# Optimization experiments

Measured on AMD Instinct MI355X. Metric: run time of the kernel, lower is better.

Reference implementation:

```python
import jax, jax.numpy as jnp
import numpy as np

B = 8192      # sessions
L = 64        # tokens per session
T = B * L     # total tokens
H = 128       # hidden_size
MAX_LEN = 64  # position_emb has MAX_LEN+1 rows


def setup_inputs() -> dict:
    key = jax.random.key(0)
    ks = jax.random.split(key, 10)
    s1 = 1.0 / np.sqrt(H)
    s2 = 1.0 / np.sqrt(2 * H)
    hidden = jax.random.normal(ks[0], (T, H), jnp.float32)
    seq_len = jnp.full((B,), L, dtype=jnp.int32)
    # reversed positions 1..L within each session (<= MAX_LEN)
    reverse_pos = jnp.tile(jnp.arange(L, 0, -1, dtype=jnp.int32), B)
    return {
        "hidden": hidden,
        "pos_table": jax.random.normal(ks[1], (MAX_LEN + 1, H), jnp.float32) * 0.02,
        "W_pos_w": jax.random.normal(ks[2], (H, 2 * H), jnp.float32) * s2,
        "W_pos_b": jax.random.normal(ks[3], (H,), jnp.float32) * s2,
        "W1_w": jax.random.normal(ks[4], (H, H), jnp.float32) * s1,
        "W1_b": jax.random.normal(ks[5], (H,), jnp.float32) * s1,
        "W2_w": jax.random.normal(ks[6], (H, H), jnp.float32) * s1,
        "W2_b": jax.random.normal(ks[7], (H,), jnp.float32) * s1,
        "q_w": jax.random.normal(ks[8], (1, H), jnp.float32) * s1,
        "q_b": jax.random.normal(ks[9], (1,), jnp.float32) * s1,
        "seq_len": seq_len,
        "reverse_pos": reverse_pos,
    }


def reference(hidden, pos_table, W_pos_w, W_pos_b, W1_w, W1_b, W2_w, W2_b,
              q_w, q_b, seq_len, reverse_pos):
    Bn = seq_len.shape[0]
    Tn = hidden.shape[0]
    # token -> session id (replaces the python split loop)
    seg = jnp.repeat(jnp.arange(Bn), seq_len, total_repeat_length=Tn)  # [T]
    # per-session mean, broadcast back to tokens (v_mean_repeat_concat)
    mean = jax.ops.segment_sum(hidden, seg, num_segments=Bn) \
        / seq_len[:, None].astype(hidden.dtype)                        # [B,H]
    mean_rep = mean[seg]                                               # [T,H]
    pos_emb = pos_table[reverse_pos]                                   # [T,H]
    pos_hidden = jnp.tanh(
        jnp.concatenate([hidden, pos_emb], axis=-1) @ W_pos_w.T + W_pos_b
    )                                                                  # [T,H]
    gate = jax.nn.sigmoid(mean_rep @ W1_w.T + W1_b + pos_hidden @ W2_w.T + W2_b)
    alpha = gate @ q_w.T + q_b                                         # [T,1]
    # per-session sum of alpha-weighted tokens (h_s)
    return jax.ops.segment_sum(alpha * hidden, seg, num_segments=Bn)   # [B,H]
```

## Files before the change

kernel.cpp:

```cpp
#include <hip/hip_runtime.h>
#include <hip/hip_bf16.h>

typedef unsigned short u16;
typedef __bf16 bf16x8 __attribute__((ext_vector_type(8)));
typedef float  f32x4  __attribute__((ext_vector_type(4)));

__device__ __forceinline__ unsigned pk2(float a, float b) {
    __hip_bfloat162 h = __float22bfloat162_rn(make_float2(a, b));
    unsigned u; __builtin_memcpy(&u, &h, 4);
    return u;
}
__device__ __forceinline__ u16 f2b1(float f) { return (u16)(pk2(f, f) & 0xFFFFu); }

#define MFMA __builtin_amdgcn_mfma_f32_16x16x32_bf16

__global__ __launch_bounds__(128) void prep_kernel(
    const float* __restrict__ pos_table, const float* __restrict__ Wpw,
    const float* __restrict__ Wpb, const float* __restrict__ W2,
    float* __restrict__ ppK, u16* __restrict__ wb1, u16* __restrict__ wb2)
{
    const int b = blockIdx.x, t = threadIdx.x;
    if (b < 65) {
        const float4* pr = (const float4*)(pos_table + b * 128);
        const float4* wr = (const float4*)(Wpw + t * 256 + 128);
        float acc = Wpb[t];
        #pragma unroll
        for (int k = 0; k < 32; ++k) {
            const float4 p = pr[k], wv = wr[k];
            acc += p.x * wv.x + p.y * wv.y + p.z * wv.z + p.w * wv.w;
        }
        ppK[b * 128 + t] = acc * 2.885390081777927f;
    } else {
        const int j = b - 65;
        wb1[j * 128 + t] = f2b1(Wpw[j * 256 + t]);
        wb2[j * 128 + t] = f2b1(W2[j * 128 + t]);
    }
}

__global__ __launch_bounds__(256, 2) void fused_kernel(
    const float* __restrict__ hidden, const int* __restrict__ rpos,
    const float* __restrict__ W1, const float* __restrict__ W1b,
    const float* __restrict__ W2b, const float* __restrict__ qw,
    const float* __restrict__ qb, const float* __restrict__ ppK,
    const u16* __restrict__ wb1g, const u16* __restrict__ wb2g,
    float* __restrict__ out)
{
    __shared__ __align__(16) u16 hbf[128 * 136];
    __shared__ __align__(16) u16 wb[128 * 136];
    __shared__ float meanv[256];
    __shared__ float g1s[256];
    __shared__ float qws[128];
    __shared__ float alphas[128];
    __shared__ int   rps[128];

    const int tid = threadIdx.x;
    const int blk = blockIdx.x;
    const int w = tid >> 6;
    const int l = tid & 63;
    const int c = l & 15;
    const int g = l >> 4;
    const int R = 32 * w;
    const float* hsrc = hidden + (size_t)blk * (128 * 128);

    meanv[tid] = 0.f;
    if (tid < 128) { rps[tid] = rpos[blk * 128 + tid]; qws[tid] = qw[tid]; }
    __syncthreads();

    {
        float4 ms0 = {0.f, 0.f, 0.f, 0.f}, ms1 = {0.f, 0.f, 0.f, 0.f};
        #pragma unroll
        for (int i = 0; i < 16; ++i) {
            const int i4 = tid + i * 256;
            const float4 v = ((const float4*)hsrc)[i4];
            const int e = i4 * 4, row = e >> 7, col = e & 127;
            uint2 st; st.x = pk2(v.x, v.y); st.y = pk2(v.z, v.w);
            *(uint2*)&hbf[row * 136 + col] = st;
            if (i < 8) { ms0.x += v.x; ms0.y += v.y; ms0.z += v.z; ms0.w += v.w; }
            else       { ms1.x += v.x; ms1.y += v.y; ms1.z += v.z; ms1.w += v.w; }
        }
        const int mc = (tid * 4) & 127;
        atomicAdd(&meanv[mc],           ms0.x); atomicAdd(&meanv[mc + 1],       ms0.y);
        atomicAdd(&meanv[mc + 2],       ms0.z); atomicAdd(&meanv[mc + 3],       ms0.w);
        atomicAdd(&meanv[128 + mc],     ms1.x); atomicAdd(&meanv[128 + mc + 1], ms1.y);
        atomicAdd(&meanv[128 + mc + 2], ms1.z); atomicAdd(&meanv[128 + mc + 3], ms1.w);
    }
    #pragma unroll
    for (int i = 0; i < 8; ++i) {
        const int ch = tid + i * 256;
        const int e = ch * 8, row = e >> 7, col = e & 127;
        *(uint4*)&wb[row * 136 + col] = ((const uint4*)wb1g)[ch];
    }
    __syncthreads();

    {
        const int col = tid & 127, s = tid >> 7;
        const float4* wr = (const float4*)(W1 + col * 128);
        const float4* mv = (const float4*)(meanv + s * 128);
        float acc = 0.f;
        #pragma unroll 8
        for (int k4 = 0; k4 < 32; ++k4) {
            const float4 wv = wr[k4], m4 = mv[k4];
            acc += m4.x * wv.x + m4.y * wv.y + m4.z * wv.z + m4.w * wv.w;
        }
        g1s[tid] = W1b[col] + W2b[col] + acc * (1.f / 64.f);
    }

    bf16x8 af[2][4];
    #pragma unroll
    for (int m = 0; m < 2; ++m)
        #pragma unroll
        for (int kk = 0; kk < 4; ++kk)
            af[m][kk] = *(const bf16x8*)&hbf[(R + 16 * m + c) * 136 + kk * 32 + g * 8];
    f32x4 acc1[2][8] = {};
    #pragma unroll
    for (int n = 0; n < 8; ++n) {
        #pragma unroll
        for (int kk = 0; kk < 4; ++kk) {
            const bf16x8 bfr = *(const bf16x8*)&wb[(16 * n + c) * 136 + kk * 32 + g * 8];
            acc1[0][n] = MFMA(af[0][kk], bfr, acc1[0][n], 0, 0, 0);
            acc1[1][n] = MFMA(af[1][kk], bfr, acc1[1][n], 0, 0, 0);
        }
    }
    {
        const float K2 = 2.885390081777927f;
        const float* pkp[2][4];
        #pragma unroll
        for (int m = 0; m < 2; ++m)
            #pragma unroll
            for (int r = 0; r < 4; ++r)
                pkp[m][r] = ppK + rps[R + 16 * m + 4 * g + r] * 128 + c;
        #pragma unroll
        for (int m = 0; m < 2; ++m)
            #pragma unroll
            for (int n = 0; n < 8; ++n)
                #pragma unroll
                for (int r = 0; r < 4; ++r) {
                    const float arg = fmaf(acc1[m][n][r], K2, pkp[m][r][16 * n]);
                    const float e2 = __builtin_amdgcn_exp2f(arg);
                    const float rc = __builtin_amdgcn_rcpf(e2 + 1.f);
                    const float th = fmaf(-2.f, rc, 1.f);
                    hbf[(R + 16 * m + 4 * g + r) * 136 + 16 * n + c] = f2b1(th);
                }
    }
    __syncthreads();

    bf16x8 af2[2][4];
    #pragma unroll
    for (int m = 0; m < 2; ++m)
        #pragma unroll
        for (int kk = 0; kk < 4; ++kk)
            af2[m][kk] = *(const bf16x8*)&hbf[(R + 16 * m + c) * 136 + kk * 32 + g * 8];
    #pragma unroll
    for (int i = 0; i < 8; ++i) {
        const int ch = tid + i * 256;
        const int e = ch * 8, row = e >> 7, col = e & 127;
        *(uint4*)&wb[row * 136 + col] = ((const uint4*)wb2g)[ch];
    }
    __syncthreads();

    f32x4 acc2[2][8] = {};
    #pragma unroll
    for (int n = 0; n < 8; ++n) {
        #pragma unroll
        for (int kk = 0; kk < 4; ++kk) {
            const bf16x8 bfr = *(const bf16x8*)&wb[(16 * n + c) * 136 + kk * 32 + g * 8];
            acc2[0][n] = MFMA(af2[0][kk], bfr, acc2[0][n], 0, 0, 0);
            acc2[1][n] = MFMA(af2[1][kk], bfr, acc2[1][n], 0, 0, 0);
        }
    }
    {
        const float K1 = 1.4426950408889634f;
        const int sw = w >> 1;
        float garr[8], qarr[8];
        #pragma unroll
        for (int n = 0; n < 8; ++n) {
            garr[n] = -K1 * g1s[sw * 128 + 16 * n + c];
            qarr[n] = qws[16 * n + c];
        }
        float prt[2][4] = {};
        #pragma unroll
        for (int m = 0; m < 2; ++m)
            #pragma unroll
            for (int n = 0; n < 8; ++n)
                #pragma unroll
                for (int r = 0; r < 4; ++r) {
                    const float arg = fmaf(acc2[m][n][r], -K1, garr[n]);
                    const float e2 = __builtin_amdgcn_exp2f(arg);
                    const float rc = __builtin_amdgcn_rcpf(e2 + 1.f);
                    prt[m][r] = fmaf(rc, qarr[n], prt[m][r]);
                }
        #pragma unroll
        for (int msk = 1; msk <= 8; msk <<= 1)
            #pragma unroll
            for (int m = 0; m < 2; ++m)
                #pragma unroll
                for (int r = 0; r < 4; ++r)
                    prt[m][r] += __shfl_xor(prt[m][r], msk, 64);
        if (c == 0) {
            const float qbv = qb[0];
            #pragma unroll
            for (int m = 0; m < 2; ++m)
                #pragma unroll
                for (int r = 0; r < 4; ++r)
                    alphas[R + 16 * m + 4 * g + r] = prt[m][r] + qbv;
        }
    }
    __syncthreads();

    {
        const int h = tid & 127, p = tid >> 7;
        const float* hs = hsrc + p * (64 * 128) + h;
        float accf = 0.f;
        #pragma unroll 8
        for (int t = 0; t < 64; ++t)
            accf = fmaf(alphas[64 * p + t], hs[t * 128], accf);
        out[(size_t)blk * 256 + tid] = accf;
    }
}

extern "C" void kernel_launch(void* const* d_in, const int* in_sizes, int n_in,
                              void* d_out, int out_size, void* d_ws, size_t ws_size,
                              hipStream_t stream)
{
    const float* hidden    = (const float*)d_in[0];
    const float* pos_table = (const float*)d_in[1];
    const float* Wpw       = (const float*)d_in[2];
    const float* Wpb       = (const float*)d_in[3];
    const float* W1w       = (const float*)d_in[4];
    const float* W1b       = (const float*)d_in[5];
    const float* W2w       = (const float*)d_in[6];
    const float* W2b       = (const float*)d_in[7];
    const float* qw        = (const float*)d_in[8];
    const float* qb        = (const float*)d_in[9];
    const int*   rpos      = (const int*)d_in[11];
    float* out = (float*)d_out;

    const int B = in_sizes[10];

    char* wsb = (char*)d_ws;
    float* ppK = (float*)wsb;
    u16* wb1   = (u16*)(wsb + 33280);
    u16* wb2   = (u16*)(wsb + 33280 + 32768);

    prep_kernel<<<193, 128, 0, stream>>>(pos_table, Wpw, Wpb, W2w,
                                         ppK, wb1, wb2);
    fused_kernel<<<B / 2, 256, 0, stream>>>(hidden, rpos, W1w, W1b, W2b, qw, qb,
                                            ppK, wb1, wb2, out);
}
```

Measured before the change: 486.2 us.

## Double threads per block to 512 with 16-row MFMA tiles per wave

Raises the fused kernel block from 256 to 512 threads (8 waves), so each wave owns 16 token rows instead of 32 and per-thread register arrays shrink. The final weighted reduction is split into half-sessions and combined through shared memory. The mean accumulation uses a wave shuffle before fewer LDS atomics, and W2 bf16 weights are prefetched into registers early rather than loaded after the first GEMM. The aim is more latency hiding and occupancy; the cost is one extra barrier and more threads contending for the same LDS footprint.

```diff
diff --git a/kernel.cpp b/kernel.cpp
--- a/kernel.cpp
+++ b/kernel.cpp
@@ -37,7 +37,7 @@
     }
 }
 
-__global__ __launch_bounds__(256, 2) void fused_kernel(
+__global__ __launch_bounds__(512, 4) void fused_kernel(
     const float* __restrict__ hidden, const int* __restrict__ rpos,
     const float* __restrict__ W1, const float* __restrict__ W1b,
     const float* __restrict__ W2b, const float* __restrict__ qw,
@@ -47,7 +47,7 @@
 {
     __shared__ __align__(16) u16 hbf[128 * 136];
     __shared__ __align__(16) u16 wb[128 * 136];
-    __shared__ float meanv[256];
+    __shared__ __align__(16) float scratch[512];
     __shared__ float g1s[256];
     __shared__ float qws[128];
     __shared__ float alphas[128];
@@ -59,43 +59,51 @@
     const int l = tid & 63;
     const int c = l & 15;
     const int g = l >> 4;
-    const int R = 32 * w;
+    const int R = 16 * w;
     const float* hsrc = hidden + (size_t)blk * (128 * 128);
 
-    meanv[tid] = 0.f;
+    scratch[tid] = 0.f;
     if (tid < 128) { rps[tid] = rpos[blk * 128 + tid]; qws[tid] = qw[tid]; }
     __syncthreads();
 
+    uint4 wreg[4];
     {
         float4 ms0 = {0.f, 0.f, 0.f, 0.f}, ms1 = {0.f, 0.f, 0.f, 0.f};
         #pragma unroll
-        for (int i = 0; i < 16; ++i) {
-            const int i4 = tid + i * 256;
+        for (int i = 0; i < 8; ++i) {
+            const int i4 = tid + i * 512;
             const float4 v = ((const float4*)hsrc)[i4];
-            const int e = i4 * 4, row = e >> 7, col = e & 127;
+            const int row = i4 >> 5, col = (i4 * 4) & 127;
             uint2 st; st.x = pk2(v.x, v.y); st.y = pk2(v.z, v.w);
             *(uint2*)&hbf[row * 136 + col] = st;
-            if (i < 8) { ms0.x += v.x; ms0.y += v.y; ms0.z += v.z; ms0.w += v.w; }
+            if (i < 4) { ms0.x += v.x; ms0.y += v.y; ms0.z += v.z; ms0.w += v.w; }
             else       { ms1.x += v.x; ms1.y += v.y; ms1.z += v.z; ms1.w += v.w; }
         }
-        const int mc = (tid * 4) & 127;
-        atomicAdd(&meanv[mc],           ms0.x); atomicAdd(&meanv[mc + 1],       ms0.y);
-        atomicAdd(&meanv[mc + 2],       ms0.z); atomicAdd(&meanv[mc + 3],       ms0.w);
-        atomicAdd(&meanv[128 + mc],     ms1.x); atomicAdd(&meanv[128 + mc + 1], ms1.y);
-        atomicAdd(&meanv[128 + mc + 2], ms1.z); atomicAdd(&meanv[128 + mc + 3], ms1.w);
-    }
-    #pragma unroll
-    for (int i = 0; i < 8; ++i) {
-        const int ch = tid + i * 256;
-        const int e = ch * 8, row = e >> 7, col = e & 127;
+        ms0.x += __shfl_xor(ms0.x, 32, 64); ms0.y += __shfl_xor(ms0.y, 32, 64);
+        ms0.z += __shfl_xor(ms0.z, 32, 64); ms0.w += __shfl_xor(ms0.w, 32, 64);
+        ms1.x += __shfl_xor(ms1.x, 32, 64); ms1.y += __shfl_xor(ms1.y, 32, 64);
+        ms1.z += __shfl_xor(ms1.z, 32, 64); ms1.w += __shfl_xor(ms1.w, 32, 64);
+        if (l < 32) {
+            const int mc = 4 * l;
+            atomicAdd(&scratch[mc],           ms0.x); atomicAdd(&scratch[mc + 1],       ms0.y);
+            atomicAdd(&scratch[mc + 2],       ms0.z); atomicAdd(&scratch[mc + 3],       ms0.w);
+            atomicAdd(&scratch[128 + mc],     ms1.x); atomicAdd(&scratch[128 + mc + 1], ms1.y);
+            atomicAdd(&scratch[128 + mc + 2], ms1.z); atomicAdd(&scratch[128 + mc + 3], ms1.w);
+        }
+    }
+    #pragma unroll
+    for (int i = 0; i < 4; ++i) {
+        const int ch = tid + i * 512;
+        const int row = ch >> 4, col = (ch * 8) & 127;
         *(uint4*)&wb[row * 136 + col] = ((const uint4*)wb1g)[ch];
-    }
-    __syncthreads();
-
-    {
+        wreg[i] = ((const uint4*)wb2g)[ch];
+    }
+    __syncthreads();
+
+    if (tid < 256) {
         const int col = tid & 127, s = tid >> 7;
         const float4* wr = (const float4*)(W1 + col * 128);
-        const float4* mv = (const float4*)(meanv + s * 128);
+        const float4* mv = (const float4*)(scratch + s * 128);
         float acc = 0.f;
         #pragma unroll 8
         for (int k4 = 0; k4 < 32; ++k4) {
@@ -105,117 +113,106 @@
         g1s[tid] = W1b[col] + W2b[col] + acc * (1.f / 64.f);
     }
 
-    bf16x8 af[2][4];
-    #pragma unroll
-    for (int m = 0; m < 2; ++m)
-        #pragma unroll
-        for (int kk = 0; kk < 4; ++kk)
-            af[m][kk] = *(const bf16x8*)&hbf[(R + 16 * m + c) * 136 + kk * 32 + g * 8];
-    f32x4 acc1[2][8] = {};
+    bf16x8 af[4];
+    #pragma unroll
+    for (int kk = 0; kk < 4; ++kk)
+        af[kk] = *(const bf16x8*)&hbf[(R + c) * 136 + kk * 32 + g * 8];
+    f32x4 acc1[8] = {};
     #pragma unroll
     for (int n = 0; n < 8; ++n) {
         #pragma unroll
         for (int kk = 0; kk < 4; ++kk) {
             const bf16x8 bfr = *(const bf16x8*)&wb[(16 * n + c) * 136 + kk * 32 + g * 8];
-            acc1[0][n] = MFMA(af[0][kk], bfr, acc1[0][n], 0, 0, 0);
-            acc1[1][n] = MFMA(af[1][kk], bfr, acc1[1][n], 0, 0, 0);
+            acc1[n] = MFMA(af[kk], bfr, acc1[n], 0, 0, 0);
         }
     }
     {
         const float K2 = 2.885390081777927f;
-        const float* pkp[2][4];
-        #pragma unroll
-        for (int m = 0; m < 2; ++m)
-            #pragma unroll
-            for (int r = 0; r < 4; ++r)
-                pkp[m][r] = ppK + rps[R + 16 * m + 4 * g + r] * 128 + c;
-        #pragma unroll
-        for (int m = 0; m < 2; ++m)
-            #pragma unroll
-            for (int n = 0; n < 8; ++n)
-                #pragma unroll
-                for (int r = 0; r < 4; ++r) {
-                    const float arg = fmaf(acc1[m][n][r], K2, pkp[m][r][16 * n]);
-                    const float e2 = __builtin_amdgcn_exp2f(arg);
-                    const float rc = __builtin_amdgcn_rcpf(e2 + 1.f);
-                    const float th = fmaf(-2.f, rc, 1.f);
-                    hbf[(R + 16 * m + 4 * g + r) * 136 + 16 * n + c] = f2b1(th);
-                }
-    }
-    __syncthreads();
-
-    bf16x8 af2[2][4];
-    #pragma unroll
-    for (int m = 0; m < 2; ++m)
-        #pragma unroll
-        for (int kk = 0; kk < 4; ++kk)
-            af2[m][kk] = *(const bf16x8*)&hbf[(R + 16 * m + c) * 136 + kk * 32 + g * 8];
-    #pragma unroll
-    for (int i = 0; i < 8; ++i) {
-        const int ch = tid + i * 256;
-        const int e = ch * 8, row = e >> 7, col = e & 127;
-        *(uint4*)&wb[row * 136 + col] = ((const uint4*)wb2g)[ch];
-    }
-    __syncthreads();
-
-    f32x4 acc2[2][8] = {};
+        const float* pkp[4];
+        #pragma unroll
+        for (int r = 0; r < 4; ++r)
+            pkp[r] = ppK + rps[R + 4 * g + r] * 128 + c;
+        #pragma unroll
+        for (int n = 0; n < 8; ++n)
+            #pragma unroll
+            for (int r = 0; r < 4; ++r) {
+                const float arg = fmaf(acc1[n][r], K2, pkp[r][16 * n]);
+                const float e2 = __builtin_amdgcn_exp2f(arg);
+                const float rc = __builtin_amdgcn_rcpf(e2 + 1.f);
+                const float th = fmaf(-2.f, rc, 1.f);
+                hbf[(R + 4 * g + r) * 136 + 16 * n + c] = f2b1(th);
+            }
+    }
+    __syncthreads();
+
+    bf16x8 af2[4];
+    #pragma unroll
+    for (int kk = 0; kk < 4; ++kk)
+        af2[kk] = *(const bf16x8*)&hbf[(R + c) * 136 + kk * 32 + g * 8];
+    #pragma unroll
+    for (int i = 0; i < 4; ++i) {
+        const int ch = tid + i * 512;
+        const int row = ch >> 4, col = (ch * 8) & 127;
+        *(uint4*)&wb[row * 136 + col] = wreg[i];
+    }
+    __syncthreads();
+
+    f32x4 acc2[8] = {};
     #pragma unroll
     for (int n = 0; n < 8; ++n) {
         #pragma unroll
         for (int kk = 0; kk < 4; ++kk) {
             const bf16x8 bfr = *(const bf16x8*)&wb[(16 * n + c) * 136 + kk * 32 + g * 8];
-            acc2[0][n] = MFMA(af2[0][kk], bfr, acc2[0][n], 0, 0, 0);
-            acc2[1][n] = MFMA(af2[1][kk], bfr, acc2[1][n], 0, 0, 0);
+            acc2[n] = MFMA(af2[kk], bfr, acc2[n], 0, 0, 0);
         }
     }
     {
         const float K1 = 1.4426950408889634f;
-        const int sw = w >> 1;
+        const int sw = w >> 2;
         float garr[8], qarr[8];
         #pragma unroll
         for (int n = 0; n < 8; ++n) {
             garr[n] = -K1 * g1s[sw * 128 + 16 * n + c];
             qarr[n] = qws[16 * n + c];
         }
-        float prt[2][4] = {};
-        #pragma unroll
-        for (int m = 0; m < 2; ++m)
-            #pragma unroll
-            for (int n = 0; n < 8; ++n)
-                #pragma unroll
-                for (int r = 0; r < 4; ++r) {
-                    const float arg = fmaf(acc2[m][n][r], -K1, garr[n]);
-                    const float e2 = __builtin_amdgcn_exp2f(arg);
-                    const float rc = __builtin_amdgcn_rcpf(e2 + 1.f);
-                    prt[m][r] = fmaf(rc, qarr[n], prt[m][r]);
-                }
+        float prt[4] = {};
+        #pragma unroll
+        for (int n = 0; n < 8; ++n)
+            #pragma unroll
+            for (int r = 0; r < 4; ++r) {
+                const float arg = fmaf(acc2[n][r], -K1, garr[n]);
+                const float e2 = __builtin_amdgcn_exp2f(arg);
+                const float rc = __builtin_amdgcn_rcpf(e2 + 1.f);
+                prt[r] = fmaf(rc, qarr[n], prt[r]);
+            }
         #pragma unroll
         for (int msk = 1; msk <= 8; msk <<= 1)
             #pragma unroll
-            for (int m = 0; m < 2; ++m)
-                #pragma unroll
-                for (int r = 0; r < 4; ++r)
-                    prt[m][r] += __shfl_xor(prt[m][r], msk, 64);
+            for (int r = 0; r < 4; ++r)
+                prt[r] += __shfl_xor(prt[r], msk, 64);
         if (c == 0) {
             const float qbv = qb[0];
             #pragma unroll
-            for (int m = 0; m < 2; ++m)
-                #pragma unroll
-                for (int r = 0; r < 4; ++r)
-                    alphas[R + 16 * m + 4 * g + r] = prt[m][r] + qbv;
+            for (int r = 0; r < 4; ++r)
+                alphas[R + 4 * g + r] = prt[r] + qbv;
         }
     }
     __syncthreads();
 
     {
         const int h = tid & 127, p = tid >> 7;
-        const float* hs = hsrc + p * (64 * 128) + h;
+        const int sess = p >> 1, half = p & 1;
+        const float* hs = hsrc + (sess * 64 + half * 32) * 128 + h;
+        const float* av = alphas + sess * 64 + half * 32;
         float accf = 0.f;
         #pragma unroll 8
-        for (int t = 0; t < 64; ++t)
-            accf = fmaf(alphas[64 * p + t], hs[t * 128], accf);
-        out[(size_t)blk * 256 + tid] = accf;
-    }
+        for (int t = 0; t < 32; ++t)
+            accf = fmaf(av[t], hs[t * 128], accf);
+        scratch[half * 256 + sess * 128 + h] = accf;
+    }
+    __syncthreads();
+    if (tid < 256)
+        out[(size_t)blk * 256 + tid] = scratch[tid] + scratch[256 + tid];
 }
 
 extern "C" void kernel_launch(void* const* d_in, const int* in_sizes, int n_in,
@@ -244,6 +241,6 @@
 
     prep_kernel<<<193, 128, 0, stream>>>(pos_table, Wpw, Wpb, W2w,
                                          ppK, wb1, wb2);
-    fused_kernel<<<B / 2, 256, 0, stream>>>(hidden, rpos, W1w, W1b, W2b, qw, qb,
+    fused_kernel<<<B / 2, 512, 0, stream>>>(hidden, rpos, W1w, W1b, W2b, qw, qb,
                                             ppK, wb1, wb2, out);
 }
```

Result: no change. 488.0 us (+0.4%).
